# Optimization experiments

Measured on AMD Instinct MI355X. Metric: run time of the kernel, lower is better.

The kernel has to match this reference:

```python
import jax, jax.numpy as jnp
import numpy as np

DIM = 768
HEADS = 12
HEAD_DIM = DIM // HEADS
SCALE = HEAD_DIM ** (-0.5)
BATCH = 1
SEQ = 4096


def setup_inputs() -> dict:
    key = jax.random.key(0)
    ks = jax.random.split(key, 5)
    x = jax.random.normal(ks[0], (BATCH, SEQ, DIM), dtype=jnp.float32)
    # Linear params stored (in, out) for y = x @ W + b
    w_qkv = jax.random.normal(ks[1], (DIM, 3 * DIM), dtype=jnp.float32) * (DIM ** -0.5)
    b_qkv = jnp.zeros((3 * DIM,), dtype=jnp.float32)
    w_proj = jax.random.normal(ks[2], (DIM, DIM), dtype=jnp.float32) * (DIM ** -0.5)
    b_proj = jnp.zeros((DIM,), dtype=jnp.float32)
    return {"x": x, "w_qkv": w_qkv, "b_qkv": b_qkv, "w_proj": w_proj, "b_proj": b_proj}


def reference(x, w_qkv, b_qkv, w_proj, b_proj):
    B, S, _ = x.shape
    qkv = x @ w_qkv + b_qkv                              # [B,S,3*DIM]
    qkv = qkv.reshape(B, S, 3, HEADS, HEAD_DIM)
    q, k, v = qkv[:, :, 0], qkv[:, :, 1], qkv[:, :, 2]   # [B,S,H,D]
    # scaled dot-product attention, full score matrix as in the original
    attn = jnp.einsum("bqhd,bkhd->bhqk", q * SCALE, k)   # [B,H,S,S]
    attn = jax.nn.softmax(attn, axis=-1)
    out = jnp.einsum("bhqk,bkhd->bqhd", attn, v)         # [B,S,H,D]
    out = out.reshape(B, S, DIM)
    return out @ w_proj + b_proj
```

## Files before the change

### kernel.cpp

```cpp
#include <hip/hip_runtime.h>
#include <hip/hip_bf16.h>

#define SEQ   4096
#define DIM   768
#define HEADS 12
#define NQKV  2304
#define QSCALE 0.18033688011f

#if __has_builtin(__builtin_amdgcn_exp2f)
#define EXP2(x) __builtin_amdgcn_exp2f(x)
#else
#define EXP2(x) __expf((x) * 0.69314718056f)
#endif

typedef __bf16 bf16_t;
typedef bf16_t bf16x8 __attribute__((ext_vector_type(8)));
typedef float  f32x4  __attribute__((ext_vector_type(4)));
typedef float  f32x16 __attribute__((ext_vector_type(16)));
typedef unsigned short u16;
typedef unsigned int   u32;

static __device__ __forceinline__ float bf2f(u16 v) {
    union { float f; unsigned u; } x; x.u = ((unsigned)v) << 16; return x.f;
}
static __device__ __forceinline__ u16 f2bf(float f) {
    union { float f; unsigned u; } x; x.f = f;
    unsigned r = x.u + 0x7fff + ((x.u >> 16) & 1);
    return (u16)(r >> 16);
}
static __device__ __forceinline__ u32 fbits(float f) {
    union { float f; unsigned u; } x; x.f = f; return x.u;
}
static __device__ __forceinline__ void gload_lds16(const u16* g, u16* l) {
    __builtin_amdgcn_global_load_lds(
        (const __attribute__((address_space(1))) unsigned int*)g,
        (__attribute__((address_space(3))) unsigned int*)l, 16, 0, 0);
}

static __device__ __forceinline__ int detect_f32(const u32* __restrict__ x) {
    int lane = threadIdx.x & 63;
    int cnt = 0;
#pragma unroll
    for (int i = 0; i < 8; ++i) {
        u32 w = x[lane * 8 + i];
        cnt += (((w >> 7) & 0xFF) >= 0x8F) ? 1 : 0;
    }
#pragma unroll
    for (int m = 1; m < 64; m <<= 1) cnt += __shfl_xor(cnt, m);
    return cnt >= 64;
}

__global__ __launch_bounds__(256) void prep(
    const void* __restrict__ x, const void* __restrict__ wqkv,
    const void* __restrict__ bqkv, const void* __restrict__ wproj,
    const void* __restrict__ bproj,
    u16* __restrict__ cvt, u16* __restrict__ wqkvT, u16* __restrict__ wprojT)
{
    __shared__ u16 tile[64][65];
    const bool f32 = detect_f32((const u32*)x) != 0;
    const int b = blockIdx.x;
    const int t = threadIdx.x;

    if (b < 576) {
        const void* src; u16* dst; int K, N, tx, ty;
        if (b < 432) { src = wqkv; dst = wqkvT; K = DIM; N = NQKV; tx = b % 36; ty = b / 36; }
        else { int bb = b - 432; src = wproj; dst = wprojT; K = DIM; N = DIM; tx = bb % 12; ty = bb / 12; }
        const int k0 = ty * 64, n0 = tx * 64;
#pragma unroll
        for (int i = 0; i < 16; ++i) {
            int idx = i * 256 + t;
            int r = idx >> 6, c = idx & 63;
            size_t si = (size_t)(k0 + r) * N + n0 + c;
            tile[r][c] = f32 ? f2bf(((const float*)src)[si]) : ((const u16*)src)[si];
        }
        __syncthreads();
#pragma unroll
        for (int i = 0; i < 16; ++i) {
            int idx = i * 256 + t;
            int r = idx >> 6, c = idx & 63;
            dst[(size_t)(n0 + r) * K + k0 + c] = tile[c][r];
        }
    } else {
        const int SX = SEQ * DIM, e1 = SX + NQKV;
        const int n_cvt = e1 + DIM;
        for (int i = (b - 576) * 256 + t; i < n_cvt; i += 200 * 256) {
            const void* s; int off;
            if      (i < SX) { s = x; off = i; }
            else if (i < e1) { s = bqkv; off = i - SX; }
            else             { s = bproj; off = i - e1; }
            cvt[i] = f32 ? f2bf(((const float*)s)[off]) : ((const u16*)s)[off];
        }
    }
}

template<int MODE>
__global__ __launch_bounds__(256) void gemm128(
    const u16* __restrict__ A, const u16* __restrict__ BT, const u16* __restrict__ bias,
    u16* __restrict__ C0, float* __restrict__ Cf, u16* __restrict__ VT,
    const u32* __restrict__ xdet, int M, int N, int K)
{
    __shared__ u16 a_lds[128 * 32];
    __shared__ u16 b_lds[128 * 32];

    const int t    = threadIdx.x;
    const int w    = t >> 6;
    const int lane = t & 63;
    const int l15  = lane & 15;
    const int quad = lane >> 4;
    const int wm   = w >> 1, wn = w & 1;
    const int m0   = blockIdx.y * 128, n0 = blockIdx.x * 128;

    const int srow = w * 32 + (lane >> 2);
    const int kch  = (lane & 3) * 8;
    const u16* asrc = A  + (size_t)(m0 + srow) * K + kch;
    const u16* bsrc = BT + (size_t)(n0 + srow) * K + kch;
    u16* adst = a_lds + w * 32 * 32;
    u16* bdst = b_lds + w * 32 * 32;

    f32x4 acc[4][4] = {};

    for (int kt = 0; kt < K; kt += 32) {
        __syncthreads();
        gload_lds16(asrc,          adst);
        gload_lds16(asrc + 16 * K, adst + 16 * 32);
        gload_lds16(bsrc,          bdst);
        gload_lds16(bsrc + 16 * K, bdst + 16 * 32);
        asrc += 32; bsrc += 32;
        __syncthreads();

        const u16* ab = a_lds + (wm * 64 + l15) * 32 + quad * 8;
        const u16* bb = b_lds + (wn * 64 + l15) * 32 + quad * 8;
        bf16x8 af[4], bfr[4];
#pragma unroll
        for (int i = 0; i < 4; ++i) af[i]  = *(const bf16x8*)(ab + i * 16 * 32);
#pragma unroll
        for (int j = 0; j < 4; ++j) bfr[j] = *(const bf16x8*)(bb + j * 16 * 32);
#pragma unroll
        for (int i = 0; i < 4; ++i)
#pragma unroll
            for (int j = 0; j < 4; ++j)
                acc[i][j] = __builtin_amdgcn_mfma_f32_16x16x32_bf16(af[i], bfr[j], acc[i][j], 0, 0, 0);
    }

    bool outf32 = false;
    if (MODE == 0) outf32 = detect_f32(xdet) != 0;
#pragma unroll
    for (int i = 0; i < 4; ++i)
#pragma unroll
        for (int j = 0; j < 4; ++j)
#pragma unroll
            for (int r = 0; r < 4; ++r) {
                int m = m0 + wm * 64 + i * 16 + quad * 4 + r;
                int n = n0 + wn * 64 + j * 16 + l15;
                float v = acc[i][j][r] + bf2f(bias[n]);
                if (MODE == 0) {
                    if (outf32) Cf[(size_t)m * N + n] = v;
                    else        C0[(size_t)m * N + n] = f2bf(v);
                } else {
                    if (n < 768) {
                        C0[(size_t)m * 1536 + n] = f2bf(v * QSCALE);
                    } else if (n < 1536) {
                        C0[(size_t)m * 1536 + n] = f2bf(v);
                    } else {
                        int mp = (m & ~15) | (m & 3) |
                                 (((m >> 2) & 1) << 3) | (((m >> 3) & 1) << 2);
                        VT[(size_t)(n - 1536) * SEQ + mp] = f2bf(v);
                    }
                }
            }
}

__global__ __launch_bounds__(256, 3) void attn_kernel(
    const u16* __restrict__ qk, const u16* __restrict__ vt, u16* __restrict__ out)
{
    __shared__ u16 k_lds[3][64 * 64];
    __shared__ u16 v_lds[3][64 * 64];
    __shared__ float l_red[2][2][32];

    const int t    = threadIdx.x;
    const int w    = t >> 6;
    const int lane = t & 63;
    const int l31  = lane & 31;
    const int h    = lane >> 5;
    const int wq   = w & 1;
    const int wk   = w >> 1;

    const int lin     = blockIdx.x + (blockIdx.y << 6);
    const int logical = (lin & 7) * 96 + (lin >> 3);
    const int head    = logical >> 6;
    const int q0      = (logical & 63) * 64 + wq * 32;

    const u16* qrow = qk + (size_t)(q0 + l31) * 1536 + head * 64 + h * 8;
    bf16x8 qb[4];
#pragma unroll
    for (int s = 0; s < 4; ++s) qb[s] = *(const bf16x8*)(qrow + 16 * s);

    bf16x8 ones;
#pragma unroll
    for (int j = 0; j < 8; ++j) ones[j] = (bf16_t)1.0f;

    const f32x16 fz = {};

    const int srow = 8 * w + (lane >> 3);
    const int cs   = ((lane & 7) - srow) & 7;
    const u16* kst0 = qk + 768 + head * 64 + (size_t)srow * 1536 + cs * 8;
    const u16* kst1 = kst0 + (size_t)32 * 1536;
    const u16* vst0 = vt + (size_t)head * 64 * SEQ + (size_t)srow * SEQ + cs * 8;
    const u16* vst1 = vst0 + (size_t)32 * SEQ;
    const int woff = 8 * w * 64;

    const int krow = 32 * wk + l31;

    f32x16 o0 = {}, o1 = {}, lac = {};

    auto SK = [&](u16* kd) {
        gload_lds16(kst0, kd + woff);
        gload_lds16(kst1, kd + woff + 32 * 64);
        kst0 += (size_t)64 * 1536;
        kst1 += (size_t)64 * 1536;
    };
    auto SV = [&](u16* vd) {
        gload_lds16(vst0, vd + woff);
        gload_lds16(vst1, vd + woff + 32 * 64);
        vst0 += 64;
        vst1 += 64;
    };

    auto QK = [&](const u16* kb) -> f32x16 {
        const u16* kbase = kb + krow * 64;
        bf16x8 ka0 = *(const bf16x8*)(kbase + (((0 + h + krow) & 7) * 8));
        bf16x8 ka1 = *(const bf16x8*)(kbase + (((2 + h + krow) & 7) * 8));
        bf16x8 ka2 = *(const bf16x8*)(kbase + (((4 + h + krow) & 7) * 8));
        bf16x8 ka3 = *(const bf16x8*)(kbase + (((6 + h + krow) & 7) * 8));
        __builtin_amdgcn_s_setprio(1);
        f32x16 st = __builtin_amdgcn_mfma_f32_32x32x16_bf16(ka0, qb[0], fz, 0, 0, 0);
        st = __builtin_amdgcn_mfma_f32_32x32x16_bf16(ka1, qb[1], st, 0, 0, 0);
        st = __builtin_amdgcn_mfma_f32_32x32x16_bf16(ka2, qb[2], st, 0, 0, 0);
        st = __builtin_amdgcn_mfma_f32_32x32x16_bf16(ka3, qb[3], st, 0, 0, 0);
        __builtin_amdgcn_s_setprio(0);
        return st;
    };

    auto SMPV = [&](const f32x16& st, const u16* vb) {
        u32 q32[8];
#pragma unroll
        for (int i = 0; i < 8; ++i) {
            float pe = EXP2(st[2 * i]);
            float po = EXP2(st[2 * i + 1]);
            q32[i] = __builtin_amdgcn_perm(fbits(po), fbits(pe), 0x07060302u);
        }
        union { u32 u[4]; bf16x8 v; } pf0, pf1;
#pragma unroll
        for (int i = 0; i < 4; ++i) { pf0.u[i] = q32[i]; pf1.u[i] = q32[4 + i]; }
        __builtin_amdgcn_s_setprio(1);
#pragma unroll
        for (int s2 = 0; s2 < 2; ++s2) {
            const int c = 4 * wk + 2 * s2 + h;
            bf16x8 vb0 = *(const bf16x8*)(vb + l31 * 64 + (((c + l31) & 7) * 8));
            bf16x8 vb1 = *(const bf16x8*)(vb + (32 + l31) * 64 + (((c + 32 + l31) & 7) * 8));
            const bf16x8 pv = s2 ? pf1.v : pf0.v;
            o0  = __builtin_amdgcn_mfma_f32_32x32x16_bf16(pv, vb0, o0, 0, 0, 0);
            o1  = __builtin_amdgcn_mfma_f32_32x32x16_bf16(pv, vb1, o1, 0, 0, 0);
            lac = __builtin_amdgcn_mfma_f32_32x32x16_bf16(pv, ones, lac, 0, 0, 0);
        }
        __builtin_amdgcn_s_setprio(0);
    };

    u16 *kA = &k_lds[0][0], *kB = &k_lds[1][0], *kC = &k_lds[2][0];
    u16 *vA = &v_lds[0][0], *vB = &v_lds[1][0], *vC = &v_lds[2][0];

    SK(kA);
    SV(vA);
    SK(kB);
    asm volatile("s_waitcnt vmcnt(4)" ::: "memory");
    __builtin_amdgcn_s_barrier();
    f32x16 stA = QK(kA);
    SV(vB);
    f32x16 stB;

    for (int i = 0; i < 31; ++i) {
        SK(kC);
        asm volatile("s_waitcnt vmcnt(4)" ::: "memory");
        __builtin_amdgcn_s_barrier();
        stB = QK(kB);
        SMPV(stA, vA);
        SV(vC);
        { u16* tt = kA; kA = kB; kB = kC; kC = tt; }
        { u16* tt = vA; vA = vB; vB = vC; vC = tt; }
        SK(kC);
        asm volatile("s_waitcnt vmcnt(4)" ::: "memory");
        __builtin_amdgcn_s_barrier();
        stA = QK(kB);
        SMPV(stB, vA);
        SV(vC);
        { u16* tt = kA; kA = kB; kB = kC; kC = tt; }
        { u16* tt = vA; vA = vB; vB = vC; vC = tt; }
    }
    asm volatile("s_waitcnt vmcnt(2)" ::: "memory");
    __builtin_amdgcn_s_barrier();
    stB = QK(kB);
    SMPV(stA, vA);
    { u16* tt = kA; kA = kB; kB = kC; kC = tt; }
    { u16* tt = vA; vA = vB; vB = vC; vC = tt; }
    asm volatile("s_waitcnt vmcnt(0)" ::: "memory");
    __builtin_amdgcn_s_barrier();
    SMPV(stB, vA);
    __syncthreads();

    if (l31 == 0) {
#pragma unroll
        for (int r = 0; r < 16; ++r) {
            int row = (r & 3) + 8 * (r >> 2) + 4 * h;
            l_red[wq][wk][row] = lac[r];
        }
    }
    float* scr = (wq == 0) ? (float*)&k_lds[0][0] : (float*)&v_lds[0][0];
    if (wk == 1) {
#pragma unroll
        for (int r = 0; r < 16; ++r) {
            int row = (r & 3) + 8 * (r >> 2) + 4 * h;
            scr[row * 64 + l31]      = o0[r];
            scr[row * 64 + 32 + l31] = o1[r];
        }
    }
    __syncthreads();
    if (wk == 0) {
#pragma unroll
        for (int r = 0; r < 16; ++r) {
            int row = (r & 3) + 8 * (r >> 2) + 4 * h;
            float lt   = l_red[wq][0][row] + l_red[wq][1][row];
            float invl = 1.0f / lt;
            float s0 = o0[r] + scr[row * 64 + l31];
            float s1 = o1[r] + scr[row * 64 + 32 + l31];
            size_t gr = (size_t)(q0 + row) * 768 + head * 64;
            out[gr + l31]      = f2bf(s0 * invl);
            out[gr + 32 + l31] = f2bf(s1 * invl);
        }
    }
}

extern "C" void kernel_launch(void* const* d_in, const int* in_sizes, int n_in,
                              void* d_out, int out_size, void* d_ws, size_t ws_size,
                              hipStream_t stream) {
    const int SX = SEQ * DIM;

    u16* base   = (u16*)d_ws;
    u16* xb     = base;
    u16* bqkvb  = xb + SX;
    u16* bprojb = bqkvb + NQKV;
    u16* wqkvT  = bprojb + DIM;
    u16* wprojT = wqkvT + (size_t)NQKV * DIM;
    u16* qkb    = wprojT + (size_t)DIM * DIM;
    u16* vtb    = qkb + (size_t)SEQ * 1536;
    u16* attnb  = xb;

    prep<<<776, 256, 0, stream>>>(
        d_in[0], d_in[1], d_in[2], d_in[3], d_in[4], base, wqkvT, wprojT);
    gemm128<1><<<dim3(NQKV / 128, SEQ / 128), 256, 0, stream>>>(
        xb, wqkvT, bqkvb, qkb, nullptr, vtb, (const u32*)d_in[0],
        SEQ, NQKV, DIM);
    attn_kernel<<<dim3(SEQ / 64, HEADS), 256, 0, stream>>>(qkb, vtb, attnb);
    gemm128<0><<<dim3(DIM / 128, SEQ / 128), 256, 0, stream>>>(
        attnb, wprojT, bprojb, (u16*)d_out, (float*)d_out, nullptr,
        (const u32*)d_in[0], SEQ, DIM, DIM);
}
```

Baseline: 221.7 us.

## Halve attention block to two waves each covering 64 query rows

The attention kernel now uses 128 threads (two waves) per block instead of four. Each wave holds Q fragments for all 64 query rows and computes two score tiles per K fragment, so K/V fragments read from LDS are reused across both query halves. Each wave issues four async global-to-LDS loads per tile instead of two, and the vmcnt waits are adjusted to match. This cuts LDS read traffic per MFMA. The cost is higher register pressure (six accumulators plus double score tiles) and fewer waves per CU available to hide latency.

```diff
diff --git a/kernel.cpp b/kernel.cpp
--- a/kernel.cpp
+++ b/kernel.cpp
@@ -170,30 +170,33 @@
             }
 }
 
-__global__ __launch_bounds__(256, 3) void attn_kernel(
+__global__ __launch_bounds__(128, 2) void attn_kernel(
     const u16* __restrict__ qk, const u16* __restrict__ vt, u16* __restrict__ out)
 {
     __shared__ u16 k_lds[3][64 * 64];
     __shared__ u16 v_lds[3][64 * 64];
-    __shared__ float l_red[2][2][32];
+    __shared__ float l_red[2][64];
 
     const int t    = threadIdx.x;
     const int w    = t >> 6;
     const int lane = t & 63;
     const int l31  = lane & 31;
     const int h    = lane >> 5;
-    const int wq   = w & 1;
-    const int wk   = w >> 1;
+    const int wk   = w;
 
     const int lin     = blockIdx.x + (blockIdx.y << 6);
     const int logical = (lin & 7) * 96 + (lin >> 3);
     const int head    = logical >> 6;
-    const int q0      = (logical & 63) * 64 + wq * 32;
-
-    const u16* qrow = qk + (size_t)(q0 + l31) * 1536 + head * 64 + h * 8;
-    bf16x8 qb[4];
-#pragma unroll
-    for (int s = 0; s < 4; ++s) qb[s] = *(const bf16x8*)(qrow + 16 * s);
+    const int q0      = (logical & 63) * 64;
+
+    const u16* qrow0 = qk + (size_t)(q0 + l31) * 1536 + head * 64 + h * 8;
+    const u16* qrow1 = qrow0 + (size_t)32 * 1536;
+    bf16x8 qb0[4], qb1[4];
+#pragma unroll
+    for (int s = 0; s < 4; ++s) {
+        qb0[s] = *(const bf16x8*)(qrow0 + 16 * s);
+        qb1[s] = *(const bf16x8*)(qrow1 + 16 * s);
+    }
 
     bf16x8 ones;
 #pragma unroll
@@ -201,67 +204,80 @@
 
     const f32x16 fz = {};
 
-    const int srow = 8 * w + (lane >> 3);
+    const int srow = 32 * w + (lane >> 3);
     const int cs   = ((lane & 7) - srow) & 7;
-    const u16* kst0 = qk + 768 + head * 64 + (size_t)srow * 1536 + cs * 8;
-    const u16* kst1 = kst0 + (size_t)32 * 1536;
-    const u16* vst0 = vt + (size_t)head * 64 * SEQ + (size_t)srow * SEQ + cs * 8;
-    const u16* vst1 = vst0 + (size_t)32 * SEQ;
-    const int woff = 8 * w * 64;
+    const u16* kst = qk + 768 + head * 64 + (size_t)srow * 1536 + cs * 8;
+    const u16* vst = vt + (size_t)head * 64 * SEQ + (size_t)srow * SEQ + cs * 8;
+    const int woff = 32 * w * 64;
 
     const int krow = 32 * wk + l31;
 
-    f32x16 o0 = {}, o1 = {}, lac = {};
+    f32x16 o0 = {}, o1 = {}, o2 = {}, o3 = {}, lac0 = {}, lac1 = {};
 
     auto SK = [&](u16* kd) {
-        gload_lds16(kst0, kd + woff);
-        gload_lds16(kst1, kd + woff + 32 * 64);
-        kst0 += (size_t)64 * 1536;
-        kst1 += (size_t)64 * 1536;
+        gload_lds16(kst,             kd + woff);
+        gload_lds16(kst +  8 * 1536, kd + woff +  8 * 64);
+        gload_lds16(kst + 16 * 1536, kd + woff + 16 * 64);
+        gload_lds16(kst + 24 * 1536, kd + woff + 24 * 64);
+        kst += (size_t)64 * 1536;
     };
     auto SV = [&](u16* vd) {
-        gload_lds16(vst0, vd + woff);
-        gload_lds16(vst1, vd + woff + 32 * 64);
-        vst0 += 64;
-        vst1 += 64;
+        gload_lds16(vst,            vd + woff);
+        gload_lds16(vst +  8 * SEQ, vd + woff +  8 * 64);
+        gload_lds16(vst + 16 * SEQ, vd + woff + 16 * 64);
+        gload_lds16(vst + 24 * SEQ, vd + woff + 24 * 64);
+        vst += 64;
     };
 
-    auto QK = [&](const u16* kb) -> f32x16 {
+    auto QK = [&](const u16* kb, f32x16& s0, f32x16& s1) {
         const u16* kbase = kb + krow * 64;
         bf16x8 ka0 = *(const bf16x8*)(kbase + (((0 + h + krow) & 7) * 8));
         bf16x8 ka1 = *(const bf16x8*)(kbase + (((2 + h + krow) & 7) * 8));
         bf16x8 ka2 = *(const bf16x8*)(kbase + (((4 + h + krow) & 7) * 8));
         bf16x8 ka3 = *(const bf16x8*)(kbase + (((6 + h + krow) & 7) * 8));
         __builtin_amdgcn_s_setprio(1);
-        f32x16 st = __builtin_amdgcn_mfma_f32_32x32x16_bf16(ka0, qb[0], fz, 0, 0, 0);
-        st = __builtin_amdgcn_mfma_f32_32x32x16_bf16(ka1, qb[1], st, 0, 0, 0);
-        st = __builtin_amdgcn_mfma_f32_32x32x16_bf16(ka2, qb[2], st, 0, 0, 0);
-        st = __builtin_amdgcn_mfma_f32_32x32x16_bf16(ka3, qb[3], st, 0, 0, 0);
+        s0 = __builtin_amdgcn_mfma_f32_32x32x16_bf16(ka0, qb0[0], fz, 0, 0, 0);
+        s1 = __builtin_amdgcn_mfma_f32_32x32x16_bf16(ka0, qb1[0], fz, 0, 0, 0);
+        s0 = __builtin_amdgcn_mfma_f32_32x32x16_bf16(ka1, qb0[1], s0, 0, 0, 0);
+        s1 = __builtin_amdgcn_mfma_f32_32x32x16_bf16(ka1, qb1[1], s1, 0, 0, 0);
+        s0 = __builtin_amdgcn_mfma_f32_32x32x16_bf16(ka2, qb0[2], s0, 0, 0, 0);
+        s1 = __builtin_amdgcn_mfma_f32_32x32x16_bf16(ka2, qb1[2], s1, 0, 0, 0);
+        s0 = __builtin_amdgcn_mfma_f32_32x32x16_bf16(ka3, qb0[3], s0, 0, 0, 0);
+        s1 = __builtin_amdgcn_mfma_f32_32x32x16_bf16(ka3, qb1[3], s1, 0, 0, 0);
         __builtin_amdgcn_s_setprio(0);
-        return st;
     };
 
-    auto SMPV = [&](const f32x16& st, const u16* vb) {
-        u32 q32[8];
+    auto SMPV = [&](const f32x16& s0, const f32x16& s1, const u16* vb) {
+        u32 qa[8], qc[8];
 #pragma unroll
         for (int i = 0; i < 8; ++i) {
-            float pe = EXP2(st[2 * i]);
-            float po = EXP2(st[2 * i + 1]);
-            q32[i] = __builtin_amdgcn_perm(fbits(po), fbits(pe), 0x07060302u);
-        }
-        union { u32 u[4]; bf16x8 v; } pf0, pf1;
-#pragma unroll
-        for (int i = 0; i < 4; ++i) { pf0.u[i] = q32[i]; pf1.u[i] = q32[4 + i]; }
+            float pe = EXP2(s0[2 * i]);
+            float po = EXP2(s0[2 * i + 1]);
+            qa[i] = __builtin_amdgcn_perm(fbits(po), fbits(pe), 0x07060302u);
+            float qe = EXP2(s1[2 * i]);
+            float qo = EXP2(s1[2 * i + 1]);
+            qc[i] = __builtin_amdgcn_perm(fbits(qo), fbits(qe), 0x07060302u);
+        }
+        union { u32 u[4]; bf16x8 v; } pf00, pf01, pf10, pf11;
+#pragma unroll
+        for (int i = 0; i < 4; ++i) {
+            pf00.u[i] = qa[i]; pf01.u[i] = qa[4 + i];
+            pf10.u[i] = qc[i]; pf11.u[i] = qc[4 + i];
+        }
         __builtin_amdgcn_s_setprio(1);
 #pragma unroll
         for (int s2 = 0; s2 < 2; ++s2) {
             const int c = 4 * wk + 2 * s2 + h;
             bf16x8 vb0 = *(const bf16x8*)(vb + l31 * 64 + (((c + l31) & 7) * 8));
             bf16x8 vb1 = *(const bf16x8*)(vb + (32 + l31) * 64 + (((c + 32 + l31) & 7) * 8));
-            const bf16x8 pv = s2 ? pf1.v : pf0.v;
-            o0  = __builtin_amdgcn_mfma_f32_32x32x16_bf16(pv, vb0, o0, 0, 0, 0);
-            o1  = __builtin_amdgcn_mfma_f32_32x32x16_bf16(pv, vb1, o1, 0, 0, 0);
-            lac = __builtin_amdgcn_mfma_f32_32x32x16_bf16(pv, ones, lac, 0, 0, 0);
+            const bf16x8 pvA = s2 ? pf01.v : pf00.v;
+            const bf16x8 pvB = s2 ? pf11.v : pf10.v;
+            o0   = __builtin_amdgcn_mfma_f32_32x32x16_bf16(pvA, vb0, o0, 0, 0, 0);
+            o1   = __builtin_amdgcn_mfma_f32_32x32x16_bf16(pvA, vb1, o1, 0, 0, 0);
+            o2   = __builtin_amdgcn_mfma_f32_32x32x16_bf16(pvB, vb0, o2, 0, 0, 0);
+            o3   = __builtin_amdgcn_mfma_f32_32x32x16_bf16(pvB, vb1, o3, 0, 0, 0);
+            lac0 = __builtin_amdgcn_mfma_f32_32x32x16_bf16(pvA, ones, lac0, 0, 0, 0);
+            lac1 = __builtin_amdgcn_mfma_f32_32x32x16_bf16(pvB, ones, lac1, 0, 0, 0);
         }
         __builtin_amdgcn_s_setprio(0);
     };
@@ -272,55 +288,58 @@
     SK(kA);
     SV(vA);
     SK(kB);
-    asm volatile("s_waitcnt vmcnt(4)" ::: "memory");
+    asm volatile("s_waitcnt vmcnt(8)" ::: "memory");
     __builtin_amdgcn_s_barrier();
-    f32x16 stA = QK(kA);
+    f32x16 stA0, stA1, stB0, stB1;
+    QK(kA, stA0, stA1);
     SV(vB);
-    f32x16 stB;
 
     for (int i = 0; i < 31; ++i) {
         SK(kC);
-        asm volatile("s_waitcnt vmcnt(4)" ::: "memory");
+        asm volatile("s_waitcnt vmcnt(8)" ::: "memory");
         __builtin_amdgcn_s_barrier();
-        stB = QK(kB);
-        SMPV(stA, vA);
+        QK(kB, stB0, stB1);
+        SMPV(stA0, stA1, vA);
         SV(vC);
         { u16* tt = kA; kA = kB; kB = kC; kC = tt; }
         { u16* tt = vA; vA = vB; vB = vC; vC = tt; }
         SK(kC);
-        asm volatile("s_waitcnt vmcnt(4)" ::: "memory");
+        asm volatile("s_waitcnt vmcnt(8)" ::: "memory");
         __builtin_amdgcn_s_barrier();
-        stA = QK(kB);
-        SMPV(stB, vA);
+        QK(kB, stA0, stA1);
+        SMPV(stB0, stB1, vA);
         SV(vC);
         { u16* tt = kA; kA = kB; kB = kC; kC = tt; }
         { u16* tt = vA; vA = vB; vB = vC; vC = tt; }
     }
-    asm volatile("s_waitcnt vmcnt(2)" ::: "memory");
+    asm volatile("s_waitcnt vmcnt(4)" ::: "memory");
     __builtin_amdgcn_s_barrier();
-    stB = QK(kB);
-    SMPV(stA, vA);
+    QK(kB, stB0, stB1);
+    SMPV(stA0, stA1, vA);
     { u16* tt = kA; kA = kB; kB = kC; kC = tt; }
     { u16* tt = vA; vA = vB; vB = vC; vC = tt; }
     asm volatile("s_waitcnt vmcnt(0)" ::: "memory");
     __builtin_amdgcn_s_barrier();
-    SMPV(stB, vA);
+    SMPV(stB0, stB1, vA);
     __syncthreads();
 
     if (l31 == 0) {
 #pragma unroll
         for (int r = 0; r < 16; ++r) {
             int row = (r & 3) + 8 * (r >> 2) + 4 * h;
-            l_red[wq][wk][row] = lac[r];
-        }
-    }
-    float* scr = (wq == 0) ? (float*)&k_lds[0][0] : (float*)&v_lds[0][0];
+            l_red[wk][row]      = lac0[r];
+            l_red[wk][32 + row] = lac1[r];
+        }
+    }
+    float* scr = (float*)&k_lds[0][0];
     if (wk == 1) {
 #pragma unroll
         for (int r = 0; r < 16; ++r) {
             int row = (r & 3) + 8 * (r >> 2) + 4 * h;
-            scr[row * 64 + l31]      = o0[r];
-            scr[row * 64 + 32 + l31] = o1[r];
+            scr[row * 64 + l31]             = o0[r];
+            scr[row * 64 + 32 + l31]        = o1[r];
+            scr[(32 + row) * 64 + l31]      = o2[r];
+            scr[(32 + row) * 64 + 32 + l31] = o3[r];
         }
     }
     __syncthreads();
@@ -328,13 +347,18 @@
 #pragma unroll
         for (int r = 0; r < 16; ++r) {
             int row = (r & 3) + 8 * (r >> 2) + 4 * h;
-            float lt   = l_red[wq][0][row] + l_red[wq][1][row];
-            float invl = 1.0f / lt;
+            float inv0 = 1.0f / (l_red[0][row] + l_red[1][row]);
+            float inv1 = 1.0f / (l_red[0][32 + row] + l_red[1][32 + row]);
             float s0 = o0[r] + scr[row * 64 + l31];
             float s1 = o1[r] + scr[row * 64 + 32 + l31];
-            size_t gr = (size_t)(q0 + row) * 768 + head * 64;
-            out[gr + l31]      = f2bf(s0 * invl);
-            out[gr + 32 + l31] = f2bf(s1 * invl);
+            float s2 = o2[r] + scr[(32 + row) * 64 + l31];
+            float s3 = o3[r] + scr[(32 + row) * 64 + 32 + l31];
+            size_t gr0 = (size_t)(q0 + row) * 768 + head * 64;
+            size_t gr1 = (size_t)(q0 + 32 + row) * 768 + head * 64;
+            out[gr0 + l31]      = f2bf(s0 * inv0);
+            out[gr0 + 32 + l31] = f2bf(s1 * inv0);
+            out[gr1 + l31]      = f2bf(s2 * inv1);
+            out[gr1 + 32 + l31] = f2bf(s3 * inv1);
         }
     }
 }
@@ -359,7 +383,7 @@
     gemm128<1><<<dim3(NQKV / 128, SEQ / 128), 256, 0, stream>>>(
         xb, wqkvT, bqkvb, qkb, nullptr, vtb, (const u32*)d_in[0],
         SEQ, NQKV, DIM);
-    attn_kernel<<<dim3(SEQ / 64, HEADS), 256, 0, stream>>>(qkb, vtb, attnb);
+    attn_kernel<<<dim3(SEQ / 64, HEADS), 128, 0, stream>>>(qkb, vtb, attnb);
     gemm128<0><<<dim3(DIM / 128, SEQ / 128), 256, 0, stream>>>(
         attnb, wprojT, bprojb, (u16*)d_out, (float*)d_out, nullptr,
         (const u32*)d_in[0], SEQ, DIM, DIM);
```

Result: slower. 228.8 us (+3.2%).
